# Kernel optimization log

Measured on AMD Instinct MI355X. Metric: run time of the kernel, lower is better.

## Reference

```python
import jax, jax.numpy as jnp
import numpy as np

H = 16        # num heads
NOPE = 128    # qk_nope_head_dim
ROPE = 64     # qk_rope_head_dim
VD = 128      # v_head_dim
HID = 2048    # hidden_dim
QLR = 1536    # q_lora_rank
KVLR = 512    # kv_lora_rank
B = 4
S = 1024
EPS = 1e-6


def setup_inputs() -> dict:
    key = jax.random.key(0)
    ks = jax.random.split(key, 8)
    def w(k, o, i):
        return jax.random.normal(k, (o, i), jnp.float32) * 0.02
    x = jax.random.normal(ks[0], (B * S, HID), jnp.float32)
    wq_a = w(ks[1], QLR, HID)
    w_qa_ln = jnp.ones((QLR,), jnp.float32)
    wq_b = w(ks[2], H * (NOPE + ROPE), QLR)
    wkv_a = w(ks[3], KVLR + ROPE, HID)
    w_kva_ln = jnp.ones((KVLR,), jnp.float32)
    wk_b = w(ks[4], H * NOPE, KVLR)
    wv_b = w(ks[5], H * VD, KVLR)
    wo = w(ks[6], HID, H * VD)
    # interleaved RoPE tables: [S, ROPE//2]
    pos = jnp.arange(S, dtype=jnp.float32)
    inv_freq = 1.0 / (10000.0 ** (jnp.arange(0, ROPE, 2, dtype=jnp.float32) / ROPE))
    freqs = pos[:, None] * inv_freq[None, :]
    rotary_sin = jnp.sin(freqs)
    rotary_cos = jnp.cos(freqs)
    seqstarts = jnp.arange(B + 1, dtype=jnp.int32) * S
    return dict(x=x, wq_a=wq_a, w_qa_ln=w_qa_ln, wq_b=wq_b, wkv_a=wkv_a,
                w_kva_ln=w_kva_ln, wk_b=wk_b, wv_b=wv_b, wo=wo,
                rotary_sin=rotary_sin, rotary_cos=rotary_cos, seqstarts=seqstarts)


def rmsnorm(h, w):
    return h * jax.lax.rsqrt(jnp.mean(h * h, axis=-1, keepdims=True) + EPS) * w


def rope_interleaved(t, sin, cos):
    # t: [B,S,h,ROPE]; sin/cos: [S,ROPE//2]; rotate adjacent pairs (even, odd)
    tr = t.reshape(t.shape[:-1] + (ROPE // 2, 2))
    e, o = tr[..., 0], tr[..., 1]
    s = sin[None, :, None, :]
    c = cos[None, :, None, :]
    return jnp.stack([e * c - o * s, e * s + o * c], axis=-1).reshape(t.shape)


def reference(x, wq_a, w_qa_ln, wq_b, wkv_a, w_kva_ln, wk_b, wv_b, wo,
              rotary_sin, rotary_cos, seqstarts):
    b = seqstarts.shape[0] - 1
    s = x.shape[0] // b
    # low-rank Q: hidden -> q_lora -> H*(nope+rope)
    q = rmsnorm(x @ wq_a.T, w_qa_ln) @ wq_b.T
    q = q.reshape(b, s, H, NOPE + ROPE)
    q_nope, q_pe = q[..., :NOPE], q[..., NOPE:]
    # low-rank KV: hidden -> kv_lora + rope (k_pe shared across heads)
    kv = x @ wkv_a.T
    ckv = rmsnorm(kv[:, :KVLR], w_kva_ln)
    k_pe = kv[:, KVLR:].reshape(b, s, 1, ROPE)
    k_nope = (ckv @ wk_b.T).reshape(b, s, H, NOPE)
    v = (ckv @ wv_b.T).reshape(b, s, H, VD)
    q_pe = rope_interleaved(q_pe, rotary_sin, rotary_cos)
    k_pe = rope_interleaved(k_pe, rotary_sin, rotary_cos)
    scale = 1.0 / np.sqrt(NOPE + ROPE).astype(np.float32)
    scores = (jnp.einsum('bqhd,bkhd->bhqk', q_nope, k_nope)
              + jnp.einsum('bqhd,bkjd->bhqk', q_pe, k_pe)) * scale
    causal = jnp.tril(jnp.ones((s, s), bool))
    scores = jnp.where(causal[None, None], scores, jnp.float32(-1e30))
    p = jax.nn.softmax(scores, axis=-1)
    out = jnp.einsum('bhqk,bkhd->bqhd', p, v).reshape(b * s, H * VD)
    return out @ wo.T
```

## Files before the change

kernel.cpp:

```cpp
#include <hip/hip_runtime.h>
#include <stdint.h>

typedef __bf16 bf16;
typedef __bf16 bf16x8 __attribute__((ext_vector_type(8)));
typedef float floatx4 __attribute__((ext_vector_type(4)));
typedef float floatx16 __attribute__((ext_vector_type(16)));

#define HH     16
#define DNOPE  128
#define DROPE  64
#define DV     128
#define DQK    192
#define HID    2048
#define QLR    1536
#define KVLR   512
#define BB     4
#define SS     1024
#define NTOK   4096
#define XOUTW  2176
#define EPSF   1e-6f

__device__ inline void cvt_store4(bf16* dst, float a, float b, float c, float d) {
  union { bf16 h[4]; uint2 u; } t;
  t.h[0] = (bf16)a; t.h[1] = (bf16)b; t.h[2] = (bf16)c; t.h[3] = (bf16)d;
  *(uint2*)dst = t.u;
}

__device__ inline void gl_lds16(const bf16* g, bf16* l) {
  __builtin_amdgcn_global_load_lds(
      (const __attribute__((address_space(1))) void*)g,
      (__attribute__((address_space(3))) void*)l, 16, 0, 0);
}

__global__ __launch_bounds__(256) void cvt_all(
    const float* __restrict__ x, const float* __restrict__ wq_a,
    const float* __restrict__ wkv_a, const float* __restrict__ wq_b,
    const float* __restrict__ wk_b, const float* __restrict__ wv_b,
    const float* __restrict__ wo, bf16* __restrict__ xb,
    bf16* __restrict__ wA, bf16* __restrict__ wqbb,
    bf16* __restrict__ wkvB, bf16* __restrict__ wob, float scaleq) {
  const int blk = blockIdx.x, tid = threadIdx.x;
  const float* s; bf16* d; int rel; float sc = 1.0f;
  if (blk < 8192)       { rel = blk;         s = x;    d = xb; }
  else if (blk < 11264) { rel = blk - 8192;  s = wq_a; d = wA; }
  else if (blk < 12544) {
    rel = blk - 11264;
    int i = (rel * 256 + tid) << 2;
    bf16* dd = wA + 3145728;
    if ((i >> 11) < 576) {
      float4 v = *(const float4*)(wkv_a + i);
      cvt_store4(dd + i, v.x, v.y, v.z, v.w);
    } else {
      *(uint2*)(dd + i) = make_uint2(0u, 0u);
    }
    return;
  }
  else if (blk < 17152) { rel = blk - 12544; s = wq_b; d = wqbb; sc = scaleq; }
  else if (blk < 18176) { rel = blk - 17152; s = wk_b; d = wkvB; }
  else if (blk < 19200) { rel = blk - 18176; s = wv_b; d = wkvB + 1048576; }
  else                  { rel = blk - 19200; s = wo;   d = wob; }
  int i = (rel * 256 + tid) << 2;
  float4 v = *(const float4*)(s + i);
  cvt_store4(d + i, v.x * sc, v.y * sc, v.z * sc, v.w * sc);
}

template <typename TC, int EPI>
__global__ __launch_bounds__(256) void gemm_bt_bf16(
    const bf16* __restrict__ A, const bf16* __restrict__ Bw,
    TC* __restrict__ C0, bf16* __restrict__ C1, int M, int N, int K) {
  __shared__ __align__(16) bf16 As[3][128 * 32];
  __shared__ __align__(16) bf16 Bs[3][128 * 32];
  const int tid  = threadIdx.x;
  const int wave = tid >> 6, lane = tid & 63;
  const int gx = gridDim.x;
  const int fid = blockIdx.y * gx + blockIdx.x;
  const int cpx = (gx * gridDim.y) >> 3;
  const int sid = (fid & 7) * cpx + (fid >> 3);
  const int m0 = (sid % gx) << 7, n0 = (sid / gx) << 7;
  const int quad = lane >> 4, l16 = lane & 15;
  const int wm = (wave >> 1) << 6, wn = (wave & 1) << 6;

  const int srow0 = tid >> 2, g = tid & 3;
  const int gsw = g ^ ((srow0 >> 1) & 3);
  const int d0 = srow0 * 32 + (g << 3);
  const int d1 = d0 + 64 * 32;
  const bf16* gA0 = A  + (size_t)(m0 + srow0) * K + (gsw << 3);
  const bf16* gA1 = A  + (size_t)(m0 + srow0 + 64) * K + (gsw << 3);
  const bf16* gB0 = Bw + (size_t)(n0 + srow0) * K + (gsw << 3);
  const bf16* gB1 = Bw + (size_t)(n0 + srow0 + 64) * K + (gsw << 3);

  floatx4 acc[4][4];
#pragma unroll
  for (int i = 0; i < 4; i++)
#pragma unroll
    for (int j = 0; j < 4; j++) acc[i][j] = floatx4{0.f, 0.f, 0.f, 0.f};

  const int nk = K >> 5;
  gl_lds16(gA0, As[0] + d0); gl_lds16(gA1, As[0] + d1);
  gl_lds16(gB0, Bs[0] + d0); gl_lds16(gB1, Bs[0] + d1);
  gl_lds16(gA0 + 32, As[1] + d0); gl_lds16(gA1 + 32, As[1] + d1);
  gl_lds16(gB0 + 32, Bs[1] + d0); gl_lds16(gB1 + 32, Bs[1] + d1);

  const int swr = (l16 >> 1) & 3;
  int cur = 0, nx2 = 2;
  for (int kt = 0; kt < nk; kt++) {
    if (kt + 1 < nk)
      asm volatile("s_waitcnt vmcnt(4)\n\ts_barrier" ::: "memory");
    else
      asm volatile("s_waitcnt vmcnt(0)\n\ts_barrier" ::: "memory");
    if (kt + 2 < nk) {
      const size_t kk = (size_t)(kt + 2) << 5;
      gl_lds16(gA0 + kk, As[nx2] + d0); gl_lds16(gA1 + kk, As[nx2] + d1);
      gl_lds16(gB0 + kk, Bs[nx2] + d0); gl_lds16(gB1 + kk, Bs[nx2] + d1);
    }
    __builtin_amdgcn_sched_barrier(0);

    const bf16* cA = As[cur];
    const bf16* cB = Bs[cur];
    bf16x8 af[4], bv[4];
#pragma unroll
    for (int i = 0; i < 4; i++) {
      const int r = wm + (i << 4) + l16;
      af[i] = *(const bf16x8*)&cA[r * 32 + (((quad ^ swr) & 3) << 3)];
    }
#pragma unroll
    for (int j = 0; j < 4; j++) {
      const int r = wn + (j << 4) + l16;
      bv[j] = *(const bf16x8*)&cB[r * 32 + (((quad ^ swr) & 3) << 3)];
    }
#pragma unroll
    for (int i = 0; i < 4; i++)
#pragma unroll
      for (int j = 0; j < 4; j++)
        acc[i][j] = __builtin_amdgcn_mfma_f32_16x16x32_bf16(af[i], bv[j], acc[i][j], 0, 0, 0);

    cur = (cur == 2) ? 0 : cur + 1;
    nx2 = (nx2 == 2) ? 0 : nx2 + 1;
  }

  if constexpr (EPI == 1) {
    if (n0 >= 2048) {
#pragma unroll
      for (int i = 0; i < 4; i++) {
        int gm = m0 + wm + (i << 4) + (quad << 2);
        int bb = gm >> 10, s = gm & 1023;
#pragma unroll
        for (int j = 0; j < 4; j++) {
          int gn = n0 + wn + (j << 4) + l16 - 2048;
          int hh = gn >> 7, vd = gn & 127;
          union { bf16 h4[4]; uint2 u; } pk;
#pragma unroll
          for (int r = 0; r < 4; r++) pk.h4[r] = (bf16)acc[i][j][r];
          *(uint2*)(C1 + ((((size_t)bb * HH + hh) * DV + vd) << 10) + s) = pk.u;
        }
      }
      return;
    }
  }
  const int ldc = (EPI == 1) ? 2048 : N;
#pragma unroll
  for (int i = 0; i < 4; i++)
#pragma unroll
    for (int j = 0; j < 4; j++) {
      int gn = n0 + wn + (j << 4) + l16;
#pragma unroll
      for (int r = 0; r < 4; r++) {
        int gm = m0 + wm + (i << 4) + (quad << 2) + r;
        C0[(size_t)gm * ldc + gn] = (TC)acc[i][j][r];
      }
    }
}

__global__ __launch_bounds__(256) void norm_rope(
    const bf16* __restrict__ xout, const float* __restrict__ w_qa_ln,
    const float* __restrict__ w_kva_ln, bf16* __restrict__ qln,
    bf16* __restrict__ ckv, bf16* __restrict__ kpe,
    const float* __restrict__ rsin, const float* __restrict__ rcos) {
  const int blk = blockIdx.x, tid = threadIdx.x;
  if (blk < 8192) {
    const int row = blk & 4095;
    const bool isq = blk < 4096;
    const bf16* p = xout + (size_t)row * XOUTW + (isq ? 0 : QLR);
    const float* w = isq ? w_qa_ln : w_kva_ln;
    bf16* o = isq ? (qln + (size_t)row * QLR) : (ckv + (size_t)row * KVLR);
    const int L = isq ? QLR : KVLR;
    float ss = 0.f;
    for (int c = tid << 2; c < L; c += 1024) {
      union { uint2 u; bf16 h[4]; } t;
      t.u = *(const uint2*)(p + c);
#pragma unroll
      for (int r = 0; r < 4; r++) { float v = (float)t.h[r]; ss += v * v; }
    }
#pragma unroll
    for (int off = 32; off > 0; off >>= 1) ss += __shfl_down(ss, off);
    __shared__ float red[4];
    if ((tid & 63) == 0) red[tid >> 6] = ss;
    __syncthreads();
    float rs = rsqrtf((red[0] + red[1] + red[2] + red[3]) / (float)L + EPSF);
    for (int c = tid << 2; c < L; c += 1024) {
      union { uint2 u; bf16 h[4]; } t, ot;
      t.u = *(const uint2*)(p + c);
#pragma unroll
      for (int r = 0; r < 4; r++) ot.h[r] = (bf16)((float)t.h[r] * rs * w[c + r]);
      *(uint2*)(o + c) = ot.u;
    }
  } else {
    int idx = (blk - 8192) * 256 + tid;
    int i = idx & 31, row = idx >> 5;
    int pos = row & (SS - 1);
    union { uint u; bf16 h2[2]; } t;
    t.u = *(const uint*)(xout + (size_t)row * XOUTW + QLR + KVLR + (i << 1));
    float e = (float)t.h2[0], o = (float)t.h2[1];
    float c = rcos[(pos << 5) + i], s = rsin[(pos << 5) + i];
    t.h2[0] = (bf16)(e * c - o * s);
    t.h2[1] = (bf16)(e * s + o * c);
    *(uint*)(kpe + (size_t)row * DROPE + (i << 1)) = t.u;
  }
}

__global__ void rope_q(bf16* __restrict__ q, const float* __restrict__ sin_t,
                       const float* __restrict__ cos_t) {
  int idx = blockIdx.x * 256 + threadIdx.x;
  int i = idx & 31, h = (idx >> 5) & 15, row = idx >> 9;
  int pos = row & (SS - 1);
  bf16* base = q + ((size_t)row * HH + h) * DQK + DNOPE + (i << 1);
  union { uint u; bf16 h2[2]; } t;
  t.u = *(uint*)base;
  float e = (float)t.h2[0], o = (float)t.h2[1];
  float c = cos_t[(pos << 5) + i], s = sin_t[(pos << 5) + i];
  t.h2[0] = (bf16)(e * c - o * s);
  t.h2[1] = (bf16)(e * s + o * c);
  *(uint*)base = t.u;
}

__global__ __launch_bounds__(512, 2) void attn_kernel(
    const bf16* __restrict__ q, const bf16* __restrict__ knope,
    const bf16* __restrict__ kpe, const bf16* __restrict__ vT,
    bf16* __restrict__ out) {
  const int bt = blockIdx.x;
  const int nkt = (8 - bt) << 1;
  const int h = blockIdx.y, b = blockIdx.z;
  __shared__ __align__(16) bf16 smem[40960];
  const int tid = threadIdx.x, wave = tid >> 6, lane = tid & 63;
  const int l32 = lane & 31, hi = lane >> 5;
  const int hi4 = hi << 2;
  const int tile = (wave < 4) ? bt : (7 - bt);
  const int Q0w = (tile << 7) + ((wave & 3) << 5);
  const int qg = Q0w + l32;

  const bf16 *gkn0, *gkn1, *gkp, *gvt0, *gvt1;
  {
    int c = wave << 1;
    int r = (c << 2) + (lane >> 4);
    int bi = (lane & 15) ^ (r & 15);
    gkn0 = knope + ((size_t)((b << 10) + r) * HH + h) * DNOPE + (bi << 3);
    r = ((c + 1) << 2) + (lane >> 4);
    bi = (lane & 15) ^ (r & 15);
    gkn1 = knope + ((size_t)((b << 10) + r) * HH + h) * DNOPE + (bi << 3);
    r = (wave << 3) + (lane >> 3);
    bi = (lane & 7) ^ (r & 7);
    gkp = kpe + (size_t)((b << 10) + r) * DROPE + (bi << 3);
    int dv = (wave << 4) + (lane >> 3);
    bi = (lane & 7) ^ (dv & 7);
    gvt0 = vT + ((((size_t)b * HH + h) * DV + dv) << 10) + (bi << 3);
    dv += 8;
    bi = (lane & 7) ^ (dv & 7);
    gvt1 = vT + ((((size_t)b * HH + h) * DV + dv) << 10) + (bi << 3);
  }
  const size_t knstep = (size_t)64 * HH * DNOPE;
  const size_t kpstep = (size_t)64 * DROPE;
  const int woff = wave << 10, woff2 = wave << 9;

  gl_lds16(gkn0, smem + woff);
  gl_lds16(gkn1, smem + woff + 512);
  gl_lds16(gkp,  smem + 8192 + woff2);
  gl_lds16(gvt0, smem + 12288 + woff);
  gl_lds16(gvt1, smem + 12288 + woff + 512);
  gkn0 += knstep; gkn1 += knstep; gkp += kpstep; gvt0 += 64; gvt1 += 64;

  bf16x8 qb[12];
  {
    const bf16* qbase =
        q + ((size_t)((b << 10) + Q0w + l32) * HH + h) * DQK + (hi << 3);
#pragma unroll
    for (int dc = 0; dc < 12; dc++)
      qb[dc] = *(const bf16x8*)(qbase + (dc << 4));
  }

  floatx16 acc[4];
#pragma unroll
  for (int g = 0; g < 4; g++)
#pragma unroll
    for (int r = 0; r < 16; r++) acc[g][r] = 0.f;
  float m_i = -1e30f, l_i = 0.f;

  for (int s = 0; s < nkt; s++) {
    const int k0 = s << 6;
    asm volatile("s_waitcnt vmcnt(0)\n\ts_barrier" ::: "memory");
    if (s + 1 < nkt) {
      bf16* bufp = smem + ((s + 1) & 1) * 20480;
      gl_lds16(gkn0, bufp + woff);
      gl_lds16(gkn1, bufp + woff + 512);
      gl_lds16(gkp,  bufp + 8192 + woff2);
      gl_lds16(gvt0, bufp + 12288 + woff);
      gl_lds16(gvt1, bufp + 12288 + woff + 512);
      gkn0 += knstep; gkn1 += knstep; gkp += kpstep; gvt0 += 64; gvt1 += 64;
    }
    __builtin_amdgcn_sched_barrier(0);
    if (k0 > Q0w + 31) continue;

    const bf16* Kn = smem + (s & 1) * 20480;
    const bf16* Kp = Kn + 8192;
    const bf16* Vt = Kn + 12288;

    floatx16 s0, s1;
#pragma unroll
    for (int r = 0; r < 16; r++) { s0[r] = 0.f; s1[r] = 0.f; }
    __builtin_amdgcn_s_setprio(1);
#pragma unroll
    for (int dc = 0; dc < 12; dc++) {
      bf16x8 ak0, ak1;
      if (dc < 8) {
        int gi = (((dc << 1) + hi) ^ (l32 & 15)) << 3;
        ak0 = *(const bf16x8*)&Kn[(l32 << 7) + gi];
        ak1 = *(const bf16x8*)&Kn[((32 + l32) << 7) + gi];
      } else {
        int gi = ((((dc - 8) << 1) + hi) ^ (l32 & 7)) << 3;
        ak0 = *(const bf16x8*)&Kp[(l32 << 6) + gi];
        ak1 = *(const bf16x8*)&Kp[((32 + l32) << 6) + gi];
      }
      s0 = __builtin_amdgcn_mfma_f32_32x32x16_bf16(ak0, qb[dc], s0, 0, 0, 0);
      s1 = __builtin_amdgcn_mfma_f32_32x32x16_bf16(ak1, qb[dc], s1, 0, 0, 0);
    }
    __builtin_amdgcn_s_setprio(0);

    if (k0 + 63 > Q0w) {
#pragma unroll
      for (int r = 0; r < 16; r++) {
        int rp = (r & 3) + ((r >> 2) << 3) + hi4;
        if (k0 + rp > qg)      s0[r] = -1e30f;
        if (k0 + 32 + rp > qg) s1[r] = -1e30f;
      }
    }

    float mx = -1e30f;
#pragma unroll
    for (int r = 0; r < 16; r++) mx = fmaxf(mx, fmaxf(s0[r], s1[r]));
    mx = fmaxf(mx, __shfl_xor(mx, 32));
    if (!__all(mx - m_i <= 8.0f)) {
      float mnew = fmaxf(m_i, mx);
      float alpha = exp2f(m_i - mnew);
      l_i *= alpha;
#pragma unroll
      for (int g = 0; g < 4; g++)
#pragma unroll
        for (int r = 0; r < 16; r++) acc[g][r] *= alpha;
      m_i = mnew;
    }
    float sum = 0.f;
#pragma unroll
    for (int r = 0; r < 16; r++) {
      float p0 = exp2f(s0[r] - m_i), p1 = exp2f(s1[r] - m_i);
      s0[r] = p0; s1[r] = p1;
      sum += p0 + p1;
    }
    sum += __shfl_xor(sum, 32);
    l_i += sum;

    uint P32[2][4][2];
#pragma unroll
    for (int hh = 0; hh < 4; hh++) {
      union { bf16 e[2]; uint u; } w0, w1, w2, w3;
      w0.e[0] = (bf16)s0[(hh << 2) + 0]; w0.e[1] = (bf16)s0[(hh << 2) + 1];
      w1.e[0] = (bf16)s0[(hh << 2) + 2]; w1.e[1] = (bf16)s0[(hh << 2) + 3];
      w2.e[0] = (bf16)s1[(hh << 2) + 0]; w2.e[1] = (bf16)s1[(hh << 2) + 1];
      w3.e[0] = (bf16)s1[(hh << 2) + 2]; w3.e[1] = (bf16)s1[(hh << 2) + 3];
      P32[0][hh][0] = w0.u; P32[0][hh][1] = w1.u;
      P32[1][hh][0] = w2.u; P32[1][hh][1] = w3.u;
    }
    bf16x8 bp[4];
#pragma unroll
    for (int c = 0; c < 4; c++) {
      const int t = c >> 1, sb = c & 1;
      uint send0 = hi ? P32[t][(sb << 1)][0] : P32[t][(sb << 1) + 1][0];
      uint send1 = hi ? P32[t][(sb << 1)][1] : P32[t][(sb << 1) + 1][1];
      uint r0 = __shfl_xor(send0, 32);
      uint r1 = __shfl_xor(send1, 32);
      union { uint u[4]; bf16x8 v; } f;
      if (hi == 0) {
        f.u[0] = P32[t][(sb << 1)][0]; f.u[1] = P32[t][(sb << 1)][1];
        f.u[2] = r0;                   f.u[3] = r1;
      } else {
        f.u[0] = r0;                         f.u[1] = r1;
        f.u[2] = P32[t][(sb << 1) + 1][0];   f.u[3] = P32[t][(sb << 1) + 1][1];
      }
      bp[c] = f.v;
    }

    __builtin_amdgcn_s_setprio(1);
#pragma unroll
    for (int c = 0; c < 4; c++) {
      const int gsw = (((c << 1) + hi) ^ (l32 & 7)) << 3;
#pragma unroll
      for (int g = 0; g < 4; g++) {
        bf16x8 av = *(const bf16x8*)&Vt[(((g << 5) + l32) << 6) + gsw];
        acc[g] = __builtin_amdgcn_mfma_f32_32x32x16_bf16(av, bp[c], acc[g], 0, 0, 0);
      }
    }
    __builtin_amdgcn_s_setprio(0);
  }

  const float invl = 1.0f / l_i;
  const int tok = (b << 10) + Q0w + l32;
  bf16* obase = out + ((size_t)tok * HH + h) * DV + hi4;
#pragma unroll
  for (int g = 0; g < 4; g++)
#pragma unroll
    for (int t = 0; t < 4; t++) {
      union { bf16 h4[4]; uint2 u; } pk;
#pragma unroll
      for (int r = 0; r < 4; r++)
        pk.h4[r] = (bf16)(acc[g][(t << 2) + r] * invl);
      *(uint2*)(obase + (g << 5) + (t << 3)) = pk.u;
    }
}

extern "C" void kernel_launch(void* const* d_in, const int* in_sizes, int n_in,
                              void* d_out, int out_size, void* d_ws, size_t ws_size,
                              hipStream_t stream) {
  (void)in_sizes; (void)n_in; (void)out_size; (void)ws_size;
  const float* x        = (const float*)d_in[0];
  const float* wq_a     = (const float*)d_in[1];
  const float* w_qa_ln  = (const float*)d_in[2];
  const float* wq_b     = (const float*)d_in[3];
  const float* wkv_a    = (const float*)d_in[4];
  const float* w_kva_ln = (const float*)d_in[5];
  const float* wk_b     = (const float*)d_in[6];
  const float* wv_b     = (const float*)d_in[7];
  const float* wo       = (const float*)d_in[8];
  const float* rsin     = (const float*)d_in[9];
  const float* rcos     = (const float*)d_in[10];
  float* out = (float*)d_out;

  char* ws = (char*)d_ws;
  bf16* xb    = (bf16*)(ws + 0);
  bf16* attnb = (bf16*)(ws + 0);
  bf16* xout  = (bf16*)(ws + 16777216);
  bf16* knope = (bf16*)(ws + 16777216);
  bf16* q     = (bf16*)(ws + 34603008);
  bf16* qln   = (bf16*)(ws + 59768832);
  bf16* vT    = (bf16*)(ws + 59768832);
  bf16* wA    = (bf16*)(ws + 76546048);
  bf16* wqbb  = (bf16*)(ws + 85458944);
  bf16* wkvB  = (bf16*)(ws + 94896128);
  bf16* wob   = (bf16*)(ws + 99090432);
  bf16* ckv   = (bf16*)(ws + 107479040);
  bf16* kpe   = (bf16*)(ws + 111673344);

  const float SCALEQ = (1.0f / sqrtf(192.0f)) * 1.44269504088896f;

  dim3 blk(256);
  cvt_all<<<23296, blk, 0, stream>>>(x, wq_a, wkv_a, wq_b, wk_b, wv_b, wo,
                                     xb, wA, wqbb, wkvB, wob, SCALEQ);
  gemm_bt_bf16<bf16, 0><<<dim3(32, 17), blk, 0, stream>>>(
      xb, wA, xout, nullptr, NTOK, XOUTW, HID);
  norm_rope<<<8704, blk, 0, stream>>>(xout, w_qa_ln, w_kva_ln, qln, ckv, kpe,
                                      rsin, rcos);
  gemm_bt_bf16<bf16, 0><<<dim3(32, 24), blk, 0, stream>>>(
      qln, wqbb, q, nullptr, NTOK, HH * DQK, QLR);
  rope_q<<<8192, blk, 0, stream>>>(q, rsin, rcos);
  gemm_bt_bf16<bf16, 1><<<dim3(32, 32), blk, 0, stream>>>(
      ckv, wkvB, knope, vT, NTOK, 4096, KVLR);
  attn_kernel<<<dim3(4, HH, BB), dim3(512), 0, stream>>>(
      q, knope, kpe, vT, attnb);
  gemm_bt_bf16<float, 0><<<dim3(32, 16), blk, 0, stream>>>(
      attnb, wob, out, nullptr, NTOK, HID, HID);
}
```

Baseline: 394.9 us.

## Restructure attention into 4-wave blocks with split K/V load staging

Switches the attention kernel from 512-thread blocks, each pairing two complementary causal query tiles, to 256-thread blocks that handle one 128-row query tile. The grid becomes 512 blocks, with tile order alternating by batch so heavy and light tiles mix. K/rope-K stay double-buffered, while V now uses a single buffer that is loaded at the start of each iteration and waited on with a partial vmcnt before the PV MFMAs. This overlaps the V fetch with QK and softmax and cuts LDS use, which may let more blocks share a CU. In exchange it adds a second barrier per iteration and loses the explicit causal load balancing inside each block.

```diff
diff --git a/kernel.cpp b/kernel.cpp
--- a/kernel.cpp
+++ b/kernel.cpp
@@ -233,50 +233,64 @@
   *(uint*)base = t.u;
 }
 
-__global__ __launch_bounds__(512, 2) void attn_kernel(
+__global__ __launch_bounds__(256) void attn_kernel(
     const bf16* __restrict__ q, const bf16* __restrict__ knope,
     const bf16* __restrict__ kpe, const bf16* __restrict__ vT,
     bf16* __restrict__ out) {
-  const int bt = blockIdx.x;
-  const int nkt = (8 - bt) << 1;
-  const int h = blockIdx.y, b = blockIdx.z;
-  __shared__ __align__(16) bf16 smem[40960];
+  const int id = blockIdx.x;
+  const int x = id & 7, h = (id >> 3) & 15, b = id >> 7;
+  const int qt = (b & 2) ? x : (7 - x);
+  const int nkt = (qt + 1) << 1;
+  __shared__ __align__(16) bf16 smem[32768];
   const int tid = threadIdx.x, wave = tid >> 6, lane = tid & 63;
   const int l32 = lane & 31, hi = lane >> 5;
   const int hi4 = hi << 2;
-  const int tile = (wave < 4) ? bt : (7 - bt);
-  const int Q0w = (tile << 7) + ((wave & 3) << 5);
+  const int Q0w = (qt << 7) + (wave << 5);
   const int qg = Q0w + l32;
 
-  const bf16 *gkn0, *gkn1, *gkp, *gvt0, *gvt1;
+  const bf16 *gkn0, *gkn1, *gkn2, *gkn3, *gkp0, *gkp1;
+  const bf16 *gvt0, *gvt1, *gvt2, *gvt3;
   {
-    int c = wave << 1;
-    int r = (c << 2) + (lane >> 4);
-    int bi = (lane & 15) ^ (r & 15);
-    gkn0 = knope + ((size_t)((b << 10) + r) * HH + h) * DNOPE + (bi << 3);
-    r = ((c + 1) << 2) + (lane >> 4);
-    bi = (lane & 15) ^ (r & 15);
-    gkn1 = knope + ((size_t)((b << 10) + r) * HH + h) * DNOPE + (bi << 3);
-    r = (wave << 3) + (lane >> 3);
-    bi = (lane & 7) ^ (r & 7);
-    gkp = kpe + (size_t)((b << 10) + r) * DROPE + (bi << 3);
-    int dv = (wave << 4) + (lane >> 3);
-    bi = (lane & 7) ^ (dv & 7);
-    gvt0 = vT + ((((size_t)b * HH + h) * DV + dv) << 10) + (bi << 3);
-    dv += 8;
-    bi = (lane & 7) ^ (dv & 7);
-    gvt1 = vT + ((((size_t)b * HH + h) * DV + dv) << 10) + (bi << 3);
+    const int kc = wave << 2;
+#pragma unroll
+    for (int j = 0; j < 4; j++) {
+      int r = ((kc + j) << 2) + (lane >> 4);
+      int bi = (lane & 15) ^ (r & 15);
+      const bf16* p = knope + ((size_t)((b << 10) + r) * HH + h) * DNOPE + (bi << 3);
+      if (j == 0) gkn0 = p; else if (j == 1) gkn1 = p;
+      else if (j == 2) gkn2 = p; else gkn3 = p;
+    }
+    const int pc = wave << 1;
+#pragma unroll
+    for (int j = 0; j < 2; j++) {
+      int r = ((pc + j) << 3) + (lane >> 3);
+      int bi = (lane & 7) ^ (r & 7);
+      const bf16* p = kpe + (size_t)((b << 10) + r) * DROPE + (bi << 3);
+      if (j == 0) gkp0 = p; else gkp1 = p;
+    }
+#pragma unroll
+    for (int j = 0; j < 4; j++) {
+      int dv = ((kc + j) << 3) + (lane >> 3);
+      int bi = (lane & 7) ^ (dv & 7);
+      const bf16* p = vT + ((((size_t)b * HH + h) * DV + dv) << 10) + (bi << 3);
+      if (j == 0) gvt0 = p; else if (j == 1) gvt1 = p;
+      else if (j == 2) gvt2 = p; else gvt3 = p;
+    }
   }
   const size_t knstep = (size_t)64 * HH * DNOPE;
   const size_t kpstep = (size_t)64 * DROPE;
-  const int woff = wave << 10, woff2 = wave << 9;
-
-  gl_lds16(gkn0, smem + woff);
-  gl_lds16(gkn1, smem + woff + 512);
-  gl_lds16(gkp,  smem + 8192 + woff2);
-  gl_lds16(gvt0, smem + 12288 + woff);
-  gl_lds16(gvt1, smem + 12288 + woff + 512);
-  gkn0 += knstep; gkn1 += knstep; gkp += kpstep; gvt0 += 64; gvt1 += 64;
+  const int kd = wave << 11;
+  const int pd = 8192 + (wave << 10);
+  const int vd0 = 24576 + (wave << 11);
+
+  {
+    bf16* kb = smem;
+    gl_lds16(gkn0, kb + kd);        gl_lds16(gkn1, kb + kd + 512);
+    gl_lds16(gkn2, kb + kd + 1024); gl_lds16(gkn3, kb + kd + 1536);
+    gl_lds16(gkp0, kb + pd);        gl_lds16(gkp1, kb + pd + 512);
+    gkn0 += knstep; gkn1 += knstep; gkn2 += knstep; gkn3 += knstep;
+    gkp0 += kpstep; gkp1 += kpstep;
+  }
 
   bf16x8 qb[12];
   {
@@ -297,117 +311,131 @@
   for (int s = 0; s < nkt; s++) {
     const int k0 = s << 6;
     asm volatile("s_waitcnt vmcnt(0)\n\ts_barrier" ::: "memory");
+    {
+      bf16* vb = smem;
+      gl_lds16(gvt0, vb + vd0);        gl_lds16(gvt1, vb + vd0 + 512);
+      gl_lds16(gvt2, vb + vd0 + 1024); gl_lds16(gvt3, vb + vd0 + 1536);
+      gvt0 += 64; gvt1 += 64; gvt2 += 64; gvt3 += 64;
+    }
     if (s + 1 < nkt) {
-      bf16* bufp = smem + ((s + 1) & 1) * 20480;
-      gl_lds16(gkn0, bufp + woff);
-      gl_lds16(gkn1, bufp + woff + 512);
-      gl_lds16(gkp,  bufp + 8192 + woff2);
-      gl_lds16(gvt0, bufp + 12288 + woff);
-      gl_lds16(gvt1, bufp + 12288 + woff + 512);
-      gkn0 += knstep; gkn1 += knstep; gkp += kpstep; gvt0 += 64; gvt1 += 64;
+      bf16* kb = smem + ((s + 1) & 1) * 12288;
+      gl_lds16(gkn0, kb + kd);        gl_lds16(gkn1, kb + kd + 512);
+      gl_lds16(gkn2, kb + kd + 1024); gl_lds16(gkn3, kb + kd + 1536);
+      gl_lds16(gkp0, kb + pd);        gl_lds16(gkp1, kb + pd + 512);
+      gkn0 += knstep; gkn1 += knstep; gkn2 += knstep; gkn3 += knstep;
+      gkp0 += kpstep; gkp1 += kpstep;
     }
     __builtin_amdgcn_sched_barrier(0);
-    if (k0 > Q0w + 31) continue;
-
-    const bf16* Kn = smem + (s & 1) * 20480;
-    const bf16* Kp = Kn + 8192;
-    const bf16* Vt = Kn + 12288;
-
-    floatx16 s0, s1;
-#pragma unroll
-    for (int r = 0; r < 16; r++) { s0[r] = 0.f; s1[r] = 0.f; }
-    __builtin_amdgcn_s_setprio(1);
-#pragma unroll
-    for (int dc = 0; dc < 12; dc++) {
-      bf16x8 ak0, ak1;
-      if (dc < 8) {
-        int gi = (((dc << 1) + hi) ^ (l32 & 15)) << 3;
-        ak0 = *(const bf16x8*)&Kn[(l32 << 7) + gi];
-        ak1 = *(const bf16x8*)&Kn[((32 + l32) << 7) + gi];
-      } else {
-        int gi = ((((dc - 8) << 1) + hi) ^ (l32 & 7)) << 3;
-        ak0 = *(const bf16x8*)&Kp[(l32 << 6) + gi];
-        ak1 = *(const bf16x8*)&Kp[((32 + l32) << 6) + gi];
-      }
-      s0 = __builtin_amdgcn_mfma_f32_32x32x16_bf16(ak0, qb[dc], s0, 0, 0, 0);
-      s1 = __builtin_amdgcn_mfma_f32_32x32x16_bf16(ak1, qb[dc], s1, 0, 0, 0);
-    }
-    __builtin_amdgcn_s_setprio(0);
-
-    if (k0 + 63 > Q0w) {
+
+    const bool active = (k0 <= Q0w + 31);
+    bf16x8 bp[4];
+    if (active) {
+      const bf16* Kn = smem + (s & 1) * 12288;
+      const bf16* Kp = Kn + 8192;
+
+      floatx16 s0, s1;
+#pragma unroll
+      for (int r = 0; r < 16; r++) { s0[r] = 0.f; s1[r] = 0.f; }
+      __builtin_amdgcn_s_setprio(1);
+#pragma unroll
+      for (int dc = 0; dc < 12; dc++) {
+        bf16x8 ak0, ak1;
+        if (dc < 8) {
+          int gi = (((dc << 1) + hi) ^ (l32 & 15)) << 3;
+          ak0 = *(const bf16x8*)&Kn[(l32 << 7) + gi];
+          ak1 = *(const bf16x8*)&Kn[((32 + l32) << 7) + gi];
+        } else {
+          int gi = ((((dc - 8) << 1) + hi) ^ (l32 & 7)) << 3;
+          ak0 = *(const bf16x8*)&Kp[(l32 << 6) + gi];
+          ak1 = *(const bf16x8*)&Kp[((32 + l32) << 6) + gi];
+        }
+        s0 = __builtin_amdgcn_mfma_f32_32x32x16_bf16(ak0, qb[dc], s0, 0, 0, 0);
+        s1 = __builtin_amdgcn_mfma_f32_32x32x16_bf16(ak1, qb[dc], s1, 0, 0, 0);
+      }
+      __builtin_amdgcn_s_setprio(0);
+
+      if (k0 + 63 > Q0w) {
+#pragma unroll
+        for (int r = 0; r < 16; r++) {
+          int rp = (r & 3) + ((r >> 2) << 3) + hi4;
+          if (k0 + rp > qg)      s0[r] = -1e30f;
+          if (k0 + 32 + rp > qg) s1[r] = -1e30f;
+        }
+      }
+
+      float mx = -1e30f;
+#pragma unroll
+      for (int r = 0; r < 16; r++) mx = fmaxf(mx, fmaxf(s0[r], s1[r]));
+      mx = fmaxf(mx, __shfl_xor(mx, 32));
+      if (!__all(mx - m_i <= 8.0f)) {
+        float mnew = fmaxf(m_i, mx);
+        float alpha = exp2f(m_i - mnew);
+        l_i *= alpha;
+#pragma unroll
+        for (int g = 0; g < 4; g++)
+#pragma unroll
+          for (int r = 0; r < 16; r++) acc[g][r] *= alpha;
+        m_i = mnew;
+      }
+      float sum = 0.f;
 #pragma unroll
       for (int r = 0; r < 16; r++) {
-        int rp = (r & 3) + ((r >> 2) << 3) + hi4;
-        if (k0 + rp > qg)      s0[r] = -1e30f;
-        if (k0 + 32 + rp > qg) s1[r] = -1e30f;
-      }
-    }
-
-    float mx = -1e30f;
-#pragma unroll
-    for (int r = 0; r < 16; r++) mx = fmaxf(mx, fmaxf(s0[r], s1[r]));
-    mx = fmaxf(mx, __shfl_xor(mx, 32));
-    if (!__all(mx - m_i <= 8.0f)) {
-      float mnew = fmaxf(m_i, mx);
-      float alpha = exp2f(m_i - mnew);
-      l_i *= alpha;
-#pragma unroll
-      for (int g = 0; g < 4; g++)
-#pragma unroll
-        for (int r = 0; r < 16; r++) acc[g][r] *= alpha;
-      m_i = mnew;
-    }
-    float sum = 0.f;
-#pragma unroll
-    for (int r = 0; r < 16; r++) {
-      float p0 = exp2f(s0[r] - m_i), p1 = exp2f(s1[r] - m_i);
-      s0[r] = p0; s1[r] = p1;
-      sum += p0 + p1;
-    }
-    sum += __shfl_xor(sum, 32);
-    l_i += sum;
-
-    uint P32[2][4][2];
-#pragma unroll
-    for (int hh = 0; hh < 4; hh++) {
-      union { bf16 e[2]; uint u; } w0, w1, w2, w3;
-      w0.e[0] = (bf16)s0[(hh << 2) + 0]; w0.e[1] = (bf16)s0[(hh << 2) + 1];
-      w1.e[0] = (bf16)s0[(hh << 2) + 2]; w1.e[1] = (bf16)s0[(hh << 2) + 3];
-      w2.e[0] = (bf16)s1[(hh << 2) + 0]; w2.e[1] = (bf16)s1[(hh << 2) + 1];
-      w3.e[0] = (bf16)s1[(hh << 2) + 2]; w3.e[1] = (bf16)s1[(hh << 2) + 3];
-      P32[0][hh][0] = w0.u; P32[0][hh][1] = w1.u;
-      P32[1][hh][0] = w2.u; P32[1][hh][1] = w3.u;
-    }
-    bf16x8 bp[4];
-#pragma unroll
-    for (int c = 0; c < 4; c++) {
-      const int t = c >> 1, sb = c & 1;
-      uint send0 = hi ? P32[t][(sb << 1)][0] : P32[t][(sb << 1) + 1][0];
-      uint send1 = hi ? P32[t][(sb << 1)][1] : P32[t][(sb << 1) + 1][1];
-      uint r0 = __shfl_xor(send0, 32);
-      uint r1 = __shfl_xor(send1, 32);
-      union { uint u[4]; bf16x8 v; } f;
-      if (hi == 0) {
-        f.u[0] = P32[t][(sb << 1)][0]; f.u[1] = P32[t][(sb << 1)][1];
-        f.u[2] = r0;                   f.u[3] = r1;
-      } else {
-        f.u[0] = r0;                         f.u[1] = r1;
-        f.u[2] = P32[t][(sb << 1) + 1][0];   f.u[3] = P32[t][(sb << 1) + 1][1];
-      }
-      bp[c] = f.v;
-    }
-
-    __builtin_amdgcn_s_setprio(1);
-#pragma unroll
-    for (int c = 0; c < 4; c++) {
-      const int gsw = (((c << 1) + hi) ^ (l32 & 7)) << 3;
-#pragma unroll
-      for (int g = 0; g < 4; g++) {
-        bf16x8 av = *(const bf16x8*)&Vt[(((g << 5) + l32) << 6) + gsw];
-        acc[g] = __builtin_amdgcn_mfma_f32_32x32x16_bf16(av, bp[c], acc[g], 0, 0, 0);
-      }
-    }
-    __builtin_amdgcn_s_setprio(0);
+        float p0 = exp2f(s0[r] - m_i), p1 = exp2f(s1[r] - m_i);
+        s0[r] = p0; s1[r] = p1;
+        sum += p0 + p1;
+      }
+      sum += __shfl_xor(sum, 32);
+      l_i += sum;
+
+      uint P32[2][4][2];
+#pragma unroll
+      for (int hh = 0; hh < 4; hh++) {
+        union { bf16 e[2]; uint u; } w0, w1, w2, w3;
+        w0.e[0] = (bf16)s0[(hh << 2) + 0]; w0.e[1] = (bf16)s0[(hh << 2) + 1];
+        w1.e[0] = (bf16)s0[(hh << 2) + 2]; w1.e[1] = (bf16)s0[(hh << 2) + 3];
+        w2.e[0] = (bf16)s1[(hh << 2) + 0]; w2.e[1] = (bf16)s1[(hh << 2) + 1];
+        w3.e[0] = (bf16)s1[(hh << 2) + 2]; w3.e[1] = (bf16)s1[(hh << 2) + 3];
+        P32[0][hh][0] = w0.u; P32[0][hh][1] = w1.u;
+        P32[1][hh][0] = w2.u; P32[1][hh][1] = w3.u;
+      }
+#pragma unroll
+      for (int c = 0; c < 4; c++) {
+        const int t = c >> 1, sb = c & 1;
+        uint send0 = hi ? P32[t][(sb << 1)][0] : P32[t][(sb << 1) + 1][0];
+        uint send1 = hi ? P32[t][(sb << 1)][1] : P32[t][(sb << 1) + 1][1];
+        uint r0 = __shfl_xor(send0, 32);
+        uint r1 = __shfl_xor(send1, 32);
+        union { uint u[4]; bf16x8 v; } f;
+        if (hi == 0) {
+          f.u[0] = P32[t][(sb << 1)][0]; f.u[1] = P32[t][(sb << 1)][1];
+          f.u[2] = r0;                   f.u[3] = r1;
+        } else {
+          f.u[0] = r0;                         f.u[1] = r1;
+          f.u[2] = P32[t][(sb << 1) + 1][0];   f.u[3] = P32[t][(sb << 1) + 1][1];
+        }
+        bp[c] = f.v;
+      }
+    }
+
+    if (s + 1 < nkt)
+      asm volatile("s_waitcnt vmcnt(6)\n\ts_barrier" ::: "memory");
+    else
+      asm volatile("s_waitcnt vmcnt(0)\n\ts_barrier" ::: "memory");
+
+    if (active) {
+      const bf16* Vt = smem + 24576;
+      __builtin_amdgcn_s_setprio(1);
+#pragma unroll
+      for (int c = 0; c < 4; c++) {
+        const int gsw = (((c << 1) + hi) ^ (l32 & 7)) << 3;
+#pragma unroll
+        for (int g = 0; g < 4; g++) {
+          bf16x8 av = *(const bf16x8*)&Vt[(((g << 5) + l32) << 6) + gsw];
+          acc[g] = __builtin_amdgcn_mfma_f32_32x32x16_bf16(av, bp[c], acc[g], 0, 0, 0);
+        }
+      }
+      __builtin_amdgcn_s_setprio(0);
+    }
   }
 
   const float invl = 1.0f / l_i;
@@ -471,7 +499,7 @@
   rope_q<<<8192, blk, 0, stream>>>(q, rsin, rcos);
   gemm_bt_bf16<bf16, 1><<<dim3(32, 32), blk, 0, stream>>>(
       ckv, wkvB, knope, vT, NTOK, 4096, KVLR);
-  attn_kernel<<<dim3(4, HH, BB), dim3(512), 0, stream>>>(
+  attn_kernel<<<dim3(512), dim3(256), 0, stream>>>(
       q, knope, kpe, vT, attnb);
   gemm_bt_bf16<float, 0><<<dim3(32, 16), blk, 0, stream>>>(
       attnb, wob, out, nullptr, NTOK, HID, HID);
```

After: 405.9 us. +2.8%, slower.
